# Performance work log

Measured on AMD Instinct MI355X. Metric: run time of the kernel, lower is better.

The kernel has to match this reference:

```python
import jax, jax.numpy as jnp
import numpy as np

B, C_IN, C_OUT, W, H = 8, 128, 64, 64, 64


def setup_inputs() -> dict:
    key = jax.random.key(0)
    ks = jax.random.split(key, 10)
    s_in = 1.0 / np.sqrt(C_IN)
    s_out = 1.0 / np.sqrt(C_OUT)
    return {
        "x": jax.random.normal(ks[0], (B, C_IN, W, H), dtype=jnp.float32),
        "wq": jax.random.uniform(ks[1], (C_OUT, C_IN), jnp.float32, -s_in, s_in),
        "bq": jax.random.uniform(ks[2], (C_OUT,), jnp.float32, -s_in, s_in),
        "wk": jax.random.uniform(ks[3], (C_OUT, C_IN), jnp.float32, -s_in, s_in),
        "bk": jax.random.uniform(ks[4], (C_OUT,), jnp.float32, -s_in, s_in),
        "wv": jax.random.uniform(ks[5], (C_OUT, C_IN), jnp.float32, -s_in, s_in),
        "bv": jax.random.uniform(ks[6], (C_OUT,), jnp.float32, -s_in, s_in),
        "wo": jax.random.uniform(ks[7], (C_IN, C_OUT), jnp.float32, -s_out, s_out),
        "bo": jax.random.uniform(ks[8], (C_IN,), jnp.float32, -s_out, s_out),
        "gamma": jnp.zeros((1,), dtype=jnp.float32),
    }


def reference(x, wq, bq, wk, bk, wv, bv, wo, bo, gamma):
    b, c, w, h = x.shape
    n = w * h
    x_flat = x.reshape(b, c, n)                                  # [B,C,N]
    # 1x1 Conv1d == channel matmul
    q = jnp.einsum('oc,bcn->bon', wq, x_flat) + bq[None, :, None]  # [B,Co,N]
    k = jnp.einsum('oc,bcn->bon', wk, x_flat) + bk[None, :, None]
    v = jnp.einsum('oc,bcn->bon', wv, x_flat) + bv[None, :, None]
    # attention[b, i, j] = sum_o q[b,o,i] * k[b,o,j]; scaled by sqrt(in_channels)
    scores = jnp.einsum('boi,boj->bij', q, k) / jnp.sqrt(jnp.float32(c))
    attn = jax.nn.softmax(scores, axis=-1)                        # [B,N,N]
    # out = values @ attention^T  -> out[b,o,i] = sum_j v[b,o,j] * attn[b,i,j]
    out = jnp.einsum('boj,bij->boi', v, attn)                     # [B,Co,N]
    out_c = jnp.einsum('co,bon->bcn', wo, out) + bo[None, :, None]
    return gamma[0] * out_c.reshape(b, c, w, h) + x
```

## Files before the change

kernel.cpp:

```cpp
#include <hip/hip_runtime.h>
#include <hip/hip_bf16.h>

#define B_   8
#define CIN  128
#define COUT 64
#define NPIX 4096

typedef __attribute__((ext_vector_type(8))) short short8;
typedef __attribute__((ext_vector_type(4))) short short4_t;
typedef __attribute__((ext_vector_type(4))) float f32x4;

__device__ __forceinline__ unsigned short f2bf(float f) {
    union { float f; unsigned int u; } x; x.f = f;
    return (unsigned short)((x.u + 0x7FFF + ((x.u >> 16) & 1)) >> 16);
}

__global__ __launch_bounds__(256) void w2bf_kernel(
    const float* __restrict__ wq, const float* __restrict__ wk,
    const float* __restrict__ wv, unsigned short* __restrict__ wb)
{
    const int idx = blockIdx.x * 256 + threadIdx.x;
    if (idx >= 192 * CIN) return;
    const int row = idx >> 7, c = idx & 127;
    float v;
    if (row < 64)       v = wq[row * CIN + c] * 0.08838834764831845f;
    else if (row < 128) v = wk[(row - 64) * CIN + c];
    else                v = wv[(row - 128) * CIN + c];
    wb[idx] = f2bf(v);
}

#define XRS 136
#define TRS 72

__global__ __launch_bounds__(512) void qkv_mfma_kernel(
    const float* __restrict__ x, const unsigned short* __restrict__ wb,
    const float* __restrict__ bq, const float* __restrict__ bk,
    const float* __restrict__ bv,
    unsigned short* __restrict__ qt, unsigned short* __restrict__ kt,
    unsigned short* __restrict__ vb)
{
    __shared__ __align__(16) unsigned char pool[18432];
    unsigned short* xb  = (unsigned short*)pool;
    unsigned short* trq = (unsigned short*)pool;
    unsigned short* trk = trq + 64 * TRS;

    const int n0   = blockIdx.x * 64;
    const int b    = blockIdx.y;
    const int tid  = threadIdx.x;
    const int wave = tid >> 6, lane = tid & 63;
    const int l16  = lane & 15, lh = lane >> 4;
    const int nt   = wave & 3, mh = wave >> 2;
    const float scale = 0.08838834764831845f;

    for (int i = tid; i < CIN * 64; i += 512) {
        const int c = i >> 6, n = i & 63;
        xb[n * XRS + c] = f2bf(x[((size_t)(b * CIN + c)) * NPIX + n0 + n]);
    }
    __syncthreads();

    const int n_ = nt * 16 + l16;
    short8 bx[4];
#pragma unroll
    for (int kk = 0; kk < 4; ++kk)
        bx[kk] = *(const short8*)&xb[n_ * XRS + kk * 32 + lh * 8];
    __syncthreads();

    f32x4 acc[6] = {};
#pragma unroll
    for (int m6 = 0; m6 < 6; ++m6) {
        const int mt = mh * 6 + m6;
        const unsigned short* wrow = wb + (size_t)(mt * 16 + l16) * CIN;
#pragma unroll
        for (int kk = 0; kk < 4; ++kk) {
            const short8 aw = *(const short8*)&wrow[kk * 32 + lh * 8];
            acc[m6] = __builtin_amdgcn_mfma_f32_16x16x32_bf16(aw, bx[kk], acc[m6], 0, 0, 0);
        }
    }

#pragma unroll
    for (int m6 = 0; m6 < 6; ++m6) {
        const int mt = mh * 6 + m6;
        const int o0 = (mt & 3) * 16 + lh * 4;
        if (mt < 4) {
            short4_t pk;
#pragma unroll
            for (int r = 0; r < 4; ++r) pk[r] = (short)f2bf(acc[m6][r] + bq[o0 + r] * scale);
            *(short4_t*)&trq[n_ * TRS + o0] = pk;
        } else if (mt < 8) {
            short4_t pk;
#pragma unroll
            for (int r = 0; r < 4; ++r) pk[r] = (short)f2bf(acc[m6][r] + bk[o0 + r]);
            *(short4_t*)&trk[n_ * TRS + o0] = pk;
        } else {
            const int ov = (mt - 8) * 16 + lh * 4;
#pragma unroll
            for (int r = 0; r < 4; ++r)
                vb[((size_t)(b * COUT + ov + r)) * NPIX + n0 + n_] = f2bf(acc[m6][r] + bv[ov + r]);
        }
    }
    __syncthreads();

    for (int idx = tid; idx < 1024; idx += 512) {
        const int m = idx >> 9, rem = idx & 511;
        const int row = rem >> 3, c8 = (rem & 7) * 8;
        const unsigned short* src = m ? &trk[row * TRS + c8] : &trq[row * TRS + c8];
        unsigned short* dst = m ? kt : qt;
        *(short8*)&dst[((size_t)(b * NPIX + n0 + row)) * 64 + c8] = *(const short8*)src;
    }
}

#define RS 72
#define POOL_K   0
#define POOL_V   18432
#define POOL_P   36864
#define POOL_Q   55296
#define POOL_EX  36864
#define POOL_ATT 0
#define POOL_WO  18432

__global__ __launch_bounds__(512, 4) void flash_fused_kernel(
    const unsigned short* __restrict__ qt,
    const unsigned short* __restrict__ kt,
    const unsigned short* __restrict__ vb,
    const float* __restrict__ wo, const float* __restrict__ bo,
    const float* __restrict__ gamma, const float* __restrict__ x,
    float* __restrict__ y)
{
    __shared__ __align__(16) unsigned char pool[64512];
    unsigned short* kl = (unsigned short*)(pool + POOL_K);
    unsigned short* vl = (unsigned short*)(pool + POOL_V);
    unsigned short* pl = (unsigned short*)(pool + POOL_P);
    unsigned short* ql = (unsigned short*)(pool + POOL_Q);

    const int bid  = blockIdx.x;
    const int b    = bid & 7;
    const int i0   = (bid >> 3) * 64;
    const int tid  = threadIdx.x;
    const int wave = tid >> 6, lane = tid & 63;
    const int l16  = lane & 15, lh = lane >> 4;
    const int qg   = wave & 3, jh = wave >> 2;

    {
        const int row = tid >> 3, c8 = (tid & 7) * 8;
        *(short8*)&ql[row * RS + c8] =
            *(const short8*)&qt[((size_t)(b * NPIX + i0 + row)) * 64 + c8];
    }

    short8 pre[4];
    const unsigned short* psrc[4];
    int pinc[4], pisK[4], pbuf[4], prow[4], pc8[4];
#pragma unroll
    for (int t = 0; t < 4; ++t) {
        const int cid = tid + t * 512;
        pisK[t] = (cid >> 10) == 0;
        pbuf[t] = (cid >> 9) & 1;
        prow[t] = (cid >> 3) & 63;
        pc8[t]  = (cid & 7) * 8;
        if (pisK[t]) {
            psrc[t] = kt + ((size_t)(b * NPIX + pbuf[t] * 64 + prow[t])) * 64 + pc8[t];
            pinc[t] = 2 * 64 * 64;
        } else {
            psrc[t] = vb + ((size_t)(b * COUT + prow[t])) * NPIX + pbuf[t] * 64 + pc8[t];
            pinc[t] = 2 * 64;
        }
        pre[t] = *(const short8*)psrc[t];
    }
    __syncthreads();

    const short8 aq0 = *(const short8*)&ql[(qg * 16 + l16) * RS + lh * 8];
    const short8 aq1 = *(const short8*)&ql[(qg * 16 + l16) * RS + 32 + lh * 8];

#pragma unroll
    for (int t = 0; t < 4; ++t) {
        unsigned short* dst = pisK[t] ? kl : vl;
        *(short8*)&dst[(pbuf[t] * 64 + prow[t]) * RS + pc8[t]] = pre[t];
    }
    __syncthreads();

    f32x4 acc[4] = {};
    float m_i[4] = {0.f, 0.f, 0.f, 0.f};
    float l_i[4] = {};

    const unsigned short* kbuf = kl + jh * (64 * RS);
    const unsigned short* vbuf = vl + jh * (64 * RS);

    for (int s = 0; s < 32; ++s) {
        if (s < 31) {
#pragma unroll
            for (int t = 0; t < 4; ++t) {
                psrc[t] += pinc[t];
                pre[t] = *(const short8*)psrc[t];
            }
        }
        f32x4 sv[4] = {};
#pragma unroll
        for (int js = 0; js < 4; ++js) {
            const short8 bk0 = *(const short8*)&kbuf[(js * 16 + l16) * RS + lh * 8];
            const short8 bk1 = *(const short8*)&kbuf[(js * 16 + l16) * RS + 32 + lh * 8];
            sv[js] = __builtin_amdgcn_mfma_f32_16x16x32_bf16(aq0, bk0, sv[js], 0, 0, 0);
            sv[js] = __builtin_amdgcn_mfma_f32_16x16x32_bf16(aq1, bk1, sv[js], 0, 0, 0);
        }
        float pm[4];
        bool ok = true;
#pragma unroll
        for (int r = 0; r < 4; ++r) {
            pm[r] = fmaxf(fmaxf(sv[0][r], sv[1][r]), fmaxf(sv[2][r], sv[3][r]));
            ok = ok && (pm[r] <= m_i[r] + 8.0f);
        }
        if (!__all(ok)) {
#pragma unroll
            for (int r = 0; r < 4; ++r) {
                float mx = pm[r];
                mx = fmaxf(mx, __shfl_xor(mx, 1));
                mx = fmaxf(mx, __shfl_xor(mx, 2));
                mx = fmaxf(mx, __shfl_xor(mx, 4));
                mx = fmaxf(mx, __shfl_xor(mx, 8));
                const float mnew  = fmaxf(m_i[r], mx);
                const float alpha = __expf(m_i[r] - mnew);
                l_i[r] *= alpha;
#pragma unroll
                for (int os = 0; os < 4; ++os) acc[os][r] *= alpha;
                m_i[r] = mnew;
            }
        }
#pragma unroll
        for (int r = 0; r < 4; ++r) {
            const int pr = wave * 16 + lh * 4 + r;
#pragma unroll
            for (int js = 0; js < 4; ++js) {
                const float p = __expf(sv[js][r] - m_i[r]);
                l_i[r] += p;
                pl[pr * RS + js * 16 + l16] = f2bf(p);
            }
        }
        const short8 ap0 = *(const short8*)&pl[(wave * 16 + l16) * RS + lh * 8];
        const short8 ap1 = *(const short8*)&pl[(wave * 16 + l16) * RS + 32 + lh * 8];
#pragma unroll
        for (int os = 0; os < 4; ++os) {
            const short8 bv0 = *(const short8*)&vbuf[(os * 16 + l16) * RS + lh * 8];
            const short8 bv1 = *(const short8*)&vbuf[(os * 16 + l16) * RS + 32 + lh * 8];
            acc[os] = __builtin_amdgcn_mfma_f32_16x16x32_bf16(ap0, bv0, acc[os], 0, 0, 0);
            acc[os] = __builtin_amdgcn_mfma_f32_16x16x32_bf16(ap1, bv1, acc[os], 0, 0, 0);
        }
        __syncthreads();
        if (s < 31) {
#pragma unroll
            for (int t = 0; t < 4; ++t) {
                unsigned short* dst = pisK[t] ? kl : vl;
                *(short8*)&dst[(pbuf[t] * 64 + prow[t]) * RS + pc8[t]] = pre[t];
            }
            __syncthreads();
        }
    }

    float* ex = (float*)(pool + POOL_EX);
    if (jh == 1) {
#pragma unroll
        for (int r = 0; r < 4; ++r) {
            ex[r * 256 + qg * 64 + lane]       = m_i[r];
            ex[(4 + r) * 256 + qg * 64 + lane] = l_i[r];
        }
#pragma unroll
        for (int os = 0; os < 4; ++os)
#pragma unroll
            for (int r = 0; r < 4; ++r)
                ex[(8 + os * 4 + r) * 256 + qg * 64 + lane] = acc[os][r];
    }
    __syncthreads();

    unsigned short* att = (unsigned short*)(pool + POOL_ATT);
    unsigned short* wol = (unsigned short*)(pool + POOL_WO);
    if (jh == 0) {
#pragma unroll
        for (int r = 0; r < 4; ++r) {
            const float mo = ex[r * 256 + qg * 64 + lane];
            const float lo = ex[(4 + r) * 256 + qg * 64 + lane];
            const float m  = fmaxf(m_i[r], mo);
            const float a0 = __expf(m_i[r] - m);
            const float a1 = __expf(mo - m);
            float lsum = l_i[r] * a0 + lo * a1;
#pragma unroll
            for (int os = 0; os < 4; ++os)
                acc[os][r] = acc[os][r] * a0 +
                             ex[(8 + os * 4 + r) * 256 + qg * 64 + lane] * a1;
            lsum += __shfl_xor(lsum, 1);
            lsum += __shfl_xor(lsum, 2);
            lsum += __shfl_xor(lsum, 4);
            lsum += __shfl_xor(lsum, 8);
            const float inv = 1.0f / lsum;
            const int i = qg * 16 + lh * 4 + r;
#pragma unroll
            for (int os = 0; os < 4; ++os)
                att[i * RS + os * 16 + l16] = f2bf(acc[os][r] * inv);
        }
    } else {
        for (int idx = tid - 256; idx < CIN * COUT; idx += 256) {
            const int c = idx >> 6, o = idx & 63;
            wol[c * RS + o] = f2bf(wo[idx]);
        }
    }
    __syncthreads();

    f32x4 acc2[4] = {};
#pragma unroll
    for (int kk = 0; kk < 2; ++kk) {
        const short8 aw = *(const short8*)&wol[(wave * 16 + l16) * RS + kk * 32 + lh * 8];
#pragma unroll
        for (int ns = 0; ns < 4; ++ns) {
            const short8 bt = *(const short8*)&att[(ns * 16 + l16) * RS + kk * 32 + lh * 8];
            acc2[ns] = __builtin_amdgcn_mfma_f32_16x16x32_bf16(aw, bt, acc2[ns], 0, 0, 0);
        }
    }
    const float g = gamma[0];
#pragma unroll
    for (int r = 0; r < 4; ++r) {
        const int c = wave * 16 + lh * 4 + r;
        const float bc = bo[c];
#pragma unroll
        for (int ns = 0; ns < 4; ++ns) {
            const size_t idx = ((size_t)(b * CIN + c)) * NPIX + i0 + ns * 16 + l16;
            y[idx] = g * (acc2[ns][r] + bc) + x[idx];
        }
    }
}

extern "C" void kernel_launch(void* const* d_in, const int* in_sizes, int n_in,
                              void* d_out, int out_size, void* d_ws, size_t ws_size,
                              hipStream_t stream)
{
    const float* x     = (const float*)d_in[0];
    const float* wq    = (const float*)d_in[1];
    const float* bq    = (const float*)d_in[2];
    const float* wk    = (const float*)d_in[3];
    const float* bk    = (const float*)d_in[4];
    const float* wv    = (const float*)d_in[5];
    const float* bv    = (const float*)d_in[6];
    const float* wo    = (const float*)d_in[7];
    const float* bo    = (const float*)d_in[8];
    const float* gamma = (const float*)d_in[9];
    float* out = (float*)d_out;

    const size_t plane = (size_t)B_ * NPIX * 64;
    unsigned short* qt = (unsigned short*)d_ws;
    unsigned short* kt = qt + plane;
    unsigned short* vb = kt + plane;
    unsigned short* wb = vb + plane;

    w2bf_kernel<<<dim3(96), 256, 0, stream>>>(wq, wk, wv, wb);
    qkv_mfma_kernel<<<dim3(NPIX / 64, B_), 512, 0, stream>>>(
        x, wb, bq, bk, bv, qt, kt, vb);
    flash_fused_kernel<<<dim3(512), 512, 0, stream>>>(
        qt, kt, vb, wo, bo, gamma, x, out);
}
```

Measured before the change: 174.9 us.

## Transpose QK MFMA so each lane owns one query row; shrink QKV tiles

The score MFMA operands are swapped so each lane holds the scores of a single query row. The online-softmax max and sum then reduce within the lane plus two cross-lane shuffles, replacing per-register four-step reductions, and the P tile is written as packed 4-element stores. The final merge of the two key-halves stores only one m/l value per row. Separately, the QKV projection kernel moves to 32-pixel tiles with 256 threads and float4 loads of x, and f2bf now uses the HIP intrinsic. The risks are extra shuffles to broadcast the rescale factors back to the accumulator layout, and more, smaller QKV blocks.

Result: faster. 165.0 us (-5.6%).

```diff
diff --git a/kernel.cpp b/kernel.cpp
--- a/kernel.cpp
+++ b/kernel.cpp
@@ -11,8 +11,9 @@
 typedef __attribute__((ext_vector_type(4))) float f32x4;
 
 __device__ __forceinline__ unsigned short f2bf(float f) {
-    union { float f; unsigned int u; } x; x.f = f;
-    return (unsigned short)((x.u + 0x7FFF + ((x.u >> 16) & 1)) >> 16);
+    union { __hip_bfloat16 b; unsigned short u; } c;
+    c.b = __float2bfloat16(f);
+    return c.u;
 }
 
 __global__ __launch_bounds__(256) void w2bf_kernel(
@@ -32,29 +33,33 @@
 #define XRS 136
 #define TRS 72
 
-__global__ __launch_bounds__(512) void qkv_mfma_kernel(
+__global__ __launch_bounds__(256) void qkv_mfma_kernel(
     const float* __restrict__ x, const unsigned short* __restrict__ wb,
     const float* __restrict__ bq, const float* __restrict__ bk,
     const float* __restrict__ bv,
     unsigned short* __restrict__ qt, unsigned short* __restrict__ kt,
     unsigned short* __restrict__ vb)
 {
-    __shared__ __align__(16) unsigned char pool[18432];
+    __shared__ __align__(16) unsigned char pool[9216];
     unsigned short* xb  = (unsigned short*)pool;
     unsigned short* trq = (unsigned short*)pool;
-    unsigned short* trk = trq + 64 * TRS;
-
-    const int n0   = blockIdx.x * 64;
+    unsigned short* trk = trq + 32 * TRS;
+
+    const int n0   = blockIdx.x * 32;
     const int b    = blockIdx.y;
     const int tid  = threadIdx.x;
     const int wave = tid >> 6, lane = tid & 63;
     const int l16  = lane & 15, lh = lane >> 4;
-    const int nt   = wave & 3, mh = wave >> 2;
+    const int nt   = wave & 1, mh = wave >> 1;
     const float scale = 0.08838834764831845f;
 
-    for (int i = tid; i < CIN * 64; i += 512) {
-        const int c = i >> 6, n = i & 63;
-        xb[n * XRS + c] = f2bf(x[((size_t)(b * CIN + c)) * NPIX + n0 + n]);
+    for (int i = tid; i < 1024; i += 256) {
+        const int c = i >> 3, n4 = (i & 7) * 4;
+        const float4 v4 = *(const float4*)&x[((size_t)(b * CIN + c)) * NPIX + n0 + n4];
+        xb[(n4 + 0) * XRS + c] = f2bf(v4.x);
+        xb[(n4 + 1) * XRS + c] = f2bf(v4.y);
+        xb[(n4 + 2) * XRS + c] = f2bf(v4.z);
+        xb[(n4 + 3) * XRS + c] = f2bf(v4.w);
     }
     __syncthreads();
 
@@ -100,8 +105,8 @@
     }
     __syncthreads();
 
-    for (int idx = tid; idx < 1024; idx += 512) {
-        const int m = idx >> 9, rem = idx & 511;
+    for (int idx = tid; idx < 512; idx += 256) {
+        const int m = idx >> 8, rem = idx & 255;
         const int row = rem >> 3, c8 = (rem & 7) * 8;
         const unsigned short* src = m ? &trk[row * TRS + c8] : &trq[row * TRS + c8];
         unsigned short* dst = m ? kt : qt;
@@ -114,7 +119,9 @@
 #define POOL_V   18432
 #define POOL_P   36864
 #define POOL_Q   55296
-#define POOL_EX  36864
+#define POOL_EXA 36864
+#define POOL_EXM 53248
+#define POOL_EXL 53504
 #define POOL_ATT 0
 #define POOL_WO  18432
 
@@ -148,19 +155,19 @@
 
     short8 pre[4];
     const unsigned short* psrc[4];
-    int pinc[4], pisK[4], pbuf[4], prow[4], pc8[4];
+    int pinc[4], pisK[4], pbuf[4], prw[4], pc8[4];
 #pragma unroll
     for (int t = 0; t < 4; ++t) {
         const int cid = tid + t * 512;
         pisK[t] = (cid >> 10) == 0;
         pbuf[t] = (cid >> 9) & 1;
-        prow[t] = (cid >> 3) & 63;
+        prw[t]  = (cid >> 3) & 63;
         pc8[t]  = (cid & 7) * 8;
         if (pisK[t]) {
-            psrc[t] = kt + ((size_t)(b * NPIX + pbuf[t] * 64 + prow[t])) * 64 + pc8[t];
+            psrc[t] = kt + ((size_t)(b * NPIX + pbuf[t] * 64 + prw[t])) * 64 + pc8[t];
             pinc[t] = 2 * 64 * 64;
         } else {
-            psrc[t] = vb + ((size_t)(b * COUT + prow[t])) * NPIX + pbuf[t] * 64 + pc8[t];
+            psrc[t] = vb + ((size_t)(b * COUT + prw[t])) * NPIX + pbuf[t] * 64 + pc8[t];
             pinc[t] = 2 * 64;
         }
         pre[t] = *(const short8*)psrc[t];
@@ -173,16 +180,16 @@
 #pragma unroll
     for (int t = 0; t < 4; ++t) {
         unsigned short* dst = pisK[t] ? kl : vl;
-        *(short8*)&dst[(pbuf[t] * 64 + prow[t]) * RS + pc8[t]] = pre[t];
+        *(short8*)&dst[(pbuf[t] * 64 + prw[t]) * RS + pc8[t]] = pre[t];
     }
     __syncthreads();
 
     f32x4 acc[4] = {};
-    float m_i[4] = {0.f, 0.f, 0.f, 0.f};
-    float l_i[4] = {};
+    float m_s = 0.f, l_s = 0.f;
 
     const unsigned short* kbuf = kl + jh * (64 * RS);
     const unsigned short* vbuf = vl + jh * (64 * RS);
+    const int prow = wave * 16 + l16;
 
     for (int s = 0; s < 32; ++s) {
         if (s < 31) {
@@ -197,44 +204,43 @@
         for (int js = 0; js < 4; ++js) {
             const short8 bk0 = *(const short8*)&kbuf[(js * 16 + l16) * RS + lh * 8];
             const short8 bk1 = *(const short8*)&kbuf[(js * 16 + l16) * RS + 32 + lh * 8];
-            sv[js] = __builtin_amdgcn_mfma_f32_16x16x32_bf16(aq0, bk0, sv[js], 0, 0, 0);
-            sv[js] = __builtin_amdgcn_mfma_f32_16x16x32_bf16(aq1, bk1, sv[js], 0, 0, 0);
-        }
-        float pm[4];
-        bool ok = true;
-#pragma unroll
-        for (int r = 0; r < 4; ++r) {
-            pm[r] = fmaxf(fmaxf(sv[0][r], sv[1][r]), fmaxf(sv[2][r], sv[3][r]));
-            ok = ok && (pm[r] <= m_i[r] + 8.0f);
-        }
-        if (!__all(ok)) {
+            sv[js] = __builtin_amdgcn_mfma_f32_16x16x32_bf16(bk0, aq0, sv[js], 0, 0, 0);
+            sv[js] = __builtin_amdgcn_mfma_f32_16x16x32_bf16(bk1, aq1, sv[js], 0, 0, 0);
+        }
+        float pm = sv[0][0];
+#pragma unroll
+        for (int js = 0; js < 4; ++js)
+#pragma unroll
+            for (int r = 0; r < 4; ++r) pm = fmaxf(pm, sv[js][r]);
+        if (!__all(pm <= m_s + 8.0f)) {
+            float mrow = pm;
+            mrow = fmaxf(mrow, __shfl_xor(mrow, 16));
+            mrow = fmaxf(mrow, __shfl_xor(mrow, 32));
+            const float mnew  = fmaxf(m_s, mrow);
+            const float alpha = __expf(m_s - mnew);
+            l_s *= alpha;
 #pragma unroll
             for (int r = 0; r < 4; ++r) {
-                float mx = pm[r];
-                mx = fmaxf(mx, __shfl_xor(mx, 1));
-                mx = fmaxf(mx, __shfl_xor(mx, 2));
-                mx = fmaxf(mx, __shfl_xor(mx, 4));
-                mx = fmaxf(mx, __shfl_xor(mx, 8));
-                const float mnew  = fmaxf(m_i[r], mx);
-                const float alpha = __expf(m_i[r] - mnew);
-                l_i[r] *= alpha;
-#pragma unroll
-                for (int os = 0; os < 4; ++os) acc[os][r] *= alpha;
-                m_i[r] = mnew;
+                const float ar = __shfl(alpha, lh * 4 + r);
+#pragma unroll
+                for (int os = 0; os < 4; ++os) acc[os][r] *= ar;
             }
-        }
-#pragma unroll
-        for (int r = 0; r < 4; ++r) {
-            const int pr = wave * 16 + lh * 4 + r;
-#pragma unroll
-            for (int js = 0; js < 4; ++js) {
-                const float p = __expf(sv[js][r] - m_i[r]);
-                l_i[r] += p;
-                pl[pr * RS + js * 16 + l16] = f2bf(p);
-            }
-        }
-        const short8 ap0 = *(const short8*)&pl[(wave * 16 + l16) * RS + lh * 8];
-        const short8 ap1 = *(const short8*)&pl[(wave * 16 + l16) * RS + 32 + lh * 8];
+            m_s = mnew;
+        }
+#pragma unroll
+        for (int js = 0; js < 4; ++js) {
+            const float p0 = __expf(sv[js][0] - m_s);
+            const float p1 = __expf(sv[js][1] - m_s);
+            const float p2 = __expf(sv[js][2] - m_s);
+            const float p3 = __expf(sv[js][3] - m_s);
+            l_s += (p0 + p1) + (p2 + p3);
+            short4_t pk;
+            pk[0] = (short)f2bf(p0); pk[1] = (short)f2bf(p1);
+            pk[2] = (short)f2bf(p2); pk[3] = (short)f2bf(p3);
+            *(short4_t*)&pl[prow * RS + js * 16 + lh * 4] = pk;
+        }
+        const short8 ap0 = *(const short8*)&pl[prow * RS + lh * 8];
+        const short8 ap1 = *(const short8*)&pl[prow * RS + 32 + lh * 8];
 #pragma unroll
         for (int os = 0; os < 4; ++os) {
             const short8 bv0 = *(const short8*)&vbuf[(os * 16 + l16) * RS + lh * 8];
@@ -247,51 +253,49 @@
 #pragma unroll
             for (int t = 0; t < 4; ++t) {
                 unsigned short* dst = pisK[t] ? kl : vl;
-                *(short8*)&dst[(pbuf[t] * 64 + prow[t]) * RS + pc8[t]] = pre[t];
+                *(short8*)&dst[(pbuf[t] * 64 + prw[t]) * RS + pc8[t]] = pre[t];
             }
             __syncthreads();
         }
     }
 
-    float* ex = (float*)(pool + POOL_EX);
+    l_s += __shfl_xor(l_s, 16);
+    l_s += __shfl_xor(l_s, 32);
+
+    float* exa = (float*)(pool + POOL_EXA);
+    float* exm = (float*)(pool + POOL_EXM);
+    float* exl = (float*)(pool + POOL_EXL);
     if (jh == 1) {
-#pragma unroll
-        for (int r = 0; r < 4; ++r) {
-            ex[r * 256 + qg * 64 + lane]       = m_i[r];
-            ex[(4 + r) * 256 + qg * 64 + lane] = l_i[r];
-        }
+        if (lh == 0) { exm[qg * 16 + l16] = m_s; exl[qg * 16 + l16] = l_s; }
 #pragma unroll
         for (int os = 0; os < 4; ++os)
 #pragma unroll
             for (int r = 0; r < 4; ++r)
-                ex[(8 + os * 4 + r) * 256 + qg * 64 + lane] = acc[os][r];
+                exa[(os * 4 + r) * 256 + qg * 64 + lane] = acc[os][r];
     }
     __syncthreads();
 
     unsigned short* att = (unsigned short*)(pool + POOL_ATT);
     unsigned short* wol = (unsigned short*)(pool + POOL_WO);
     if (jh == 0) {
+        const float mo = exm[qg * 16 + l16];
+        const float lo = exl[qg * 16 + l16];
+        const float m  = fmaxf(m_s, mo);
+        const float a0 = __expf(m_s - m);
+        const float a1 = __expf(mo - m);
+        const float inv = 1.0f / (l_s * a0 + lo * a1);
 #pragma unroll
         for (int r = 0; r < 4; ++r) {
-            const float mo = ex[r * 256 + qg * 64 + lane];
-            const float lo = ex[(4 + r) * 256 + qg * 64 + lane];
-            const float m  = fmaxf(m_i[r], mo);
-            const float a0 = __expf(m_i[r] - m);
-            const float a1 = __expf(mo - m);
-            float lsum = l_i[r] * a0 + lo * a1;
-#pragma unroll
-            for (int os = 0; os < 4; ++os)
-                acc[os][r] = acc[os][r] * a0 +
-                             ex[(8 + os * 4 + r) * 256 + qg * 64 + lane] * a1;
-            lsum += __shfl_xor(lsum, 1);
-            lsum += __shfl_xor(lsum, 2);
-            lsum += __shfl_xor(lsum, 4);
-            lsum += __shfl_xor(lsum, 8);
-            const float inv = 1.0f / lsum;
+            const float a0r = __shfl(a0, lh * 4 + r);
+            const float a1r = __shfl(a1, lh * 4 + r);
+            const float ivr = __shfl(inv, lh * 4 + r);
             const int i = qg * 16 + lh * 4 + r;
 #pragma unroll
-            for (int os = 0; os < 4; ++os)
-                att[i * RS + os * 16 + l16] = f2bf(acc[os][r] * inv);
+            for (int os = 0; os < 4; ++os) {
+                const float v = (acc[os][r] * a0r +
+                                 exa[(os * 4 + r) * 256 + qg * 64 + lane] * a1r) * ivr;
+                att[i * RS + os * 16 + l16] = f2bf(v);
+            }
         }
     } else {
         for (int idx = tid - 256; idx < CIN * COUT; idx += 256) {
@@ -347,7 +351,7 @@
     unsigned short* wb = vb + plane;
 
     w2bf_kernel<<<dim3(96), 256, 0, stream>>>(wq, wk, wv, wb);
-    qkv_mfma_kernel<<<dim3(NPIX / 64, B_), 512, 0, stream>>>(
+    qkv_mfma_kernel<<<dim3(NPIX / 32, B_), 256, 0, stream>>>(
         x, wb, bq, bk, bv, qt, kt, vb);
     flash_fused_kernel<<<dim3(512), 512, 0, stream>>>(
         qt, kt, vb, wo, bo, gamma, x, out);
```
